# Kernel optimization log

Measured on AMD Instinct MI355X. Metric: run time of the kernel, lower is better.

The kernel has to match this reference:

```python
import jax, jax.numpy as jnp
import numpy as np

D = 192  # volume side; H has shape [D, D, D, 3, 3]


def setup_inputs() -> dict:
    key = jax.random.key(0)
    A = jax.random.normal(key, (D, D, D, 3, 3), dtype=jnp.float32)
    # Hessians are symmetric; the analytic eigen formula assumes symmetry.
    H = 0.5 * (A + jnp.swapaxes(A, -1, -2))
    return {"H": H}


def reference(H):
    # q = trace(H)/3
    q = jnp.trace(H, axis1=-2, axis2=-1) / 3.0
    I = jnp.eye(3, dtype=H.dtype)
    C = H - q[..., None, None] * I  # deviatoric part
    # p = sqrt(||C||_F^2 / 6)
    p = jnp.sqrt(jnp.sum(C * C, axis=(-2, -1)) / 6.0)
    B = C / (p[..., None, None] + 1e-10)
    detB = jnp.linalg.det(B)
    theta = jnp.arccos(jnp.clip(detB / 2.0, -1.0, 1.0)) / 3.0
    two_pi_3 = 2.0 * np.pi / 3.0
    eig = jnp.stack(
        [2.0 * jnp.cos(theta + two_pi_3 * k) * p + q for k in range(3)], axis=-1
    )  # [..., 3]
    return jnp.sort(eig, axis=-1)
```

## Files before the change

kernel.cpp:

```cpp
#include <hip/hip_runtime.h>
#include <math.h>

#define NMAT (192*192*192)

__global__ __launch_bounds__(256) void eig3_kernel(const float* __restrict__ H,
                                                   float* __restrict__ out) {
    __shared__ float lds[256 * 9];
    const int t = threadIdx.x;
    const long long tile = blockIdx.x;
    const long long base = tile * (256LL * 9);

#pragma unroll
    for (int k = 0; k < 9; ++k)
        lds[t + 256 * k] = H[base + t + 256 * k];
    __syncthreads();

    float h[9];
#pragma unroll
    for (int j = 0; j < 9; ++j)
        h[j] = lds[t * 9 + j];
    __syncthreads();

    const float q = (h[0] + h[4] + h[8]) * (1.0f / 3.0f);
    const float c00 = h[0] - q, c01 = h[1],     c02 = h[2];
    const float c10 = h[3],     c11 = h[4] - q, c12 = h[5];
    const float c20 = h[6],     c21 = h[7],     c22 = h[8] - q;
    const float ss = c00*c00 + c01*c01 + c02*c02
                   + c10*c10 + c11*c11 + c12*c12
                   + c20*c20 + c21*c21 + c22*c22;
    const float p = sqrtf(ss * (1.0f / 6.0f));
    const float inv = 1.0f / (p + 1e-10f);
    const float b00 = c00*inv, b01 = c01*inv, b02 = c02*inv;
    const float b10 = c10*inv, b11 = c11*inv, b12 = c12*inv;
    const float b20 = c20*inv, b21 = c21*inv, b22 = c22*inv;
    const float detB = b00*(b11*b22 - b12*b21)
                     - b01*(b10*b22 - b12*b20)
                     + b02*(b10*b21 - b11*b20);
    const float x = fminf(fmaxf(detB * 0.5f, -1.0f), 1.0f);
    const float theta = acosf(x) * (1.0f / 3.0f);
    const float two_pi_3 = 2.09439510239319549f;
    const float e0 = 2.0f * cosf(theta) * p + q;
    const float e1 = 2.0f * cosf(theta + two_pi_3) * p + q;
    const float e2 = 2.0f * cosf(theta + 2.0f * two_pi_3) * p + q;

    const float a  = fminf(e0, e1), b = fmaxf(e0, e1);
    const float hi = fmaxf(b, e2),  c = fminf(b, e2);
    const float lo = fminf(a, c),   mid = fmaxf(a, c);

    lds[t * 3 + 0] = lo;
    lds[t * 3 + 1] = mid;
    lds[t * 3 + 2] = hi;
    __syncthreads();

    const long long obase = tile * (256LL * 3);
#pragma unroll
    for (int k = 0; k < 3; ++k)
        out[obase + t + 256 * k] = lds[t + 256 * k];
}

extern "C" void kernel_launch(void* const* d_in, const int* in_sizes, int n_in,
                              void* d_out, int out_size, void* d_ws, size_t ws_size,
                              hipStream_t stream) {
    const float* H = (const float*)d_in[0];
    float* out = (float*)d_out;
    const int nblocks = NMAT / 256;
    eig3_kernel<<<nblocks, 256, 0, stream>>>(H, out);
}
```

Before: 63.17 us.

## Process four matrices per thread with float4 loads and sincos eigen formula

Each block now handles 1024 matrices, staging input and output through LDS with 128-bit float4 global accesses instead of scalar loads. The three cosines are replaced by one fast __sincosf plus the angle-addition identity, cutting transcendental work. The larger LDS footprint (36KB) and more registers per thread may reduce occupancy, and __sincosf is less accurate than cosf.

```diff
diff --git a/kernel.cpp b/kernel.cpp
--- a/kernel.cpp
+++ b/kernel.cpp
@@ -2,67 +2,82 @@
 #include <math.h>
 
 #define NMAT (192*192*192)
+#define MPB  1024
 
-__global__ __launch_bounds__(256) void eig3_kernel(const float* __restrict__ H,
-                                                   float* __restrict__ out) {
-    __shared__ float lds[256 * 9];
+__global__ __launch_bounds__(256, 4) void eig3_kernel(const float4* __restrict__ H4,
+                                                      float4* __restrict__ out4) {
+    __shared__ float lds[MPB * 9];
+    float4* lds4 = (float4*)lds;
     const int t = threadIdx.x;
-    const long long tile = blockIdx.x;
-    const long long base = tile * (256LL * 9);
+    const long long blk = blockIdx.x;
+
+    const long long ibase = blk * 2304LL;
+#pragma unroll
+    for (int k = 0; k < 9; ++k)
+        lds4[t + 256 * k] = H4[ibase + t + 256 * k];
+    __syncthreads();
+
+    float res[4][3];
+#pragma unroll
+    for (int s = 0; s < 4; ++s) {
+        const int m = t + 256 * s;
+        float h[9];
+#pragma unroll
+        for (int j = 0; j < 9; ++j)
+            h[j] = lds[m * 9 + j];
+
+        const float q = (h[0] + h[4] + h[8]) * (1.0f / 3.0f);
+        const float c00 = h[0] - q, c01 = h[1],     c02 = h[2];
+        const float c10 = h[3],     c11 = h[4] - q, c12 = h[5];
+        const float c20 = h[6],     c21 = h[7],     c22 = h[8] - q;
+        const float ss = c00*c00 + c01*c01 + c02*c02
+                       + c10*c10 + c11*c11 + c12*c12
+                       + c20*c20 + c21*c21 + c22*c22;
+        const float p = sqrtf(ss * (1.0f / 6.0f));
+        const float inv = 1.0f / (p + 1e-10f);
+        const float b00 = c00*inv, b01 = c01*inv, b02 = c02*inv;
+        const float b10 = c10*inv, b11 = c11*inv, b12 = c12*inv;
+        const float b20 = c20*inv, b21 = c21*inv, b22 = c22*inv;
+        const float detB = b00*(b11*b22 - b12*b21)
+                         - b01*(b10*b22 - b12*b20)
+                         + b02*(b10*b21 - b11*b20);
+        const float x = fminf(fmaxf(detB * 0.5f, -1.0f), 1.0f);
+        const float theta = acosf(x) * (1.0f / 3.0f);
+
+        float st, ct;
+        __sincosf(theta, &st, &ct);
+        const float r3 = 1.73205080756887729f;
+        const float e0 = 2.0f * p * ct + q;
+        const float e1 = p * (-ct - r3 * st) + q;
+        const float e2 = p * (-ct + r3 * st) + q;
+
+        const float a  = fminf(e0, e1), b = fmaxf(e0, e1);
+        const float hi = fmaxf(b, e2),  c = fminf(b, e2);
+        const float lo = fminf(a, c),   mid = fmaxf(a, c);
+        res[s][0] = lo; res[s][1] = mid; res[s][2] = hi;
+    }
+    __syncthreads();
 
 #pragma unroll
-    for (int k = 0; k < 9; ++k)
-        lds[t + 256 * k] = H[base + t + 256 * k];
+    for (int s = 0; s < 4; ++s) {
+        const int m = t + 256 * s;
+        lds[m * 3 + 0] = res[s][0];
+        lds[m * 3 + 1] = res[s][1];
+        lds[m * 3 + 2] = res[s][2];
+    }
     __syncthreads();
 
-    float h[9];
-#pragma unroll
-    for (int j = 0; j < 9; ++j)
-        h[j] = lds[t * 9 + j];
-    __syncthreads();
-
-    const float q = (h[0] + h[4] + h[8]) * (1.0f / 3.0f);
-    const float c00 = h[0] - q, c01 = h[1],     c02 = h[2];
-    const float c10 = h[3],     c11 = h[4] - q, c12 = h[5];
-    const float c20 = h[6],     c21 = h[7],     c22 = h[8] - q;
-    const float ss = c00*c00 + c01*c01 + c02*c02
-                   + c10*c10 + c11*c11 + c12*c12
-                   + c20*c20 + c21*c21 + c22*c22;
-    const float p = sqrtf(ss * (1.0f / 6.0f));
-    const float inv = 1.0f / (p + 1e-10f);
-    const float b00 = c00*inv, b01 = c01*inv, b02 = c02*inv;
-    const float b10 = c10*inv, b11 = c11*inv, b12 = c12*inv;
-    const float b20 = c20*inv, b21 = c21*inv, b22 = c22*inv;
-    const float detB = b00*(b11*b22 - b12*b21)
-                     - b01*(b10*b22 - b12*b20)
-                     + b02*(b10*b21 - b11*b20);
-    const float x = fminf(fmaxf(detB * 0.5f, -1.0f), 1.0f);
-    const float theta = acosf(x) * (1.0f / 3.0f);
-    const float two_pi_3 = 2.09439510239319549f;
-    const float e0 = 2.0f * cosf(theta) * p + q;
-    const float e1 = 2.0f * cosf(theta + two_pi_3) * p + q;
-    const float e2 = 2.0f * cosf(theta + 2.0f * two_pi_3) * p + q;
-
-    const float a  = fminf(e0, e1), b = fmaxf(e0, e1);
-    const float hi = fmaxf(b, e2),  c = fminf(b, e2);
-    const float lo = fminf(a, c),   mid = fmaxf(a, c);
-
-    lds[t * 3 + 0] = lo;
-    lds[t * 3 + 1] = mid;
-    lds[t * 3 + 2] = hi;
-    __syncthreads();
-
-    const long long obase = tile * (256LL * 3);
+    const long long obase = blk * 768LL;
 #pragma unroll
     for (int k = 0; k < 3; ++k)
-        out[obase + t + 256 * k] = lds[t + 256 * k];
+        out4[obase + t + 256 * k] = lds4[t + 256 * k];
 }
 
 extern "C" void kernel_launch(void* const* d_in, const int* in_sizes, int n_in,
                               void* d_out, int out_size, void* d_ws, size_t ws_size,
                               hipStream_t stream) {
-    const float* H = (const float*)d_in[0];
-    float* out = (float*)d_out;
-    const int nblocks = NMAT / 256;
-    eig3_kernel<<<nblocks, 256, 0, stream>>>(H, out);
+    const float4* H4 = (const float4*)d_in[0];
+    float4* out4 = (float4*)d_out;
+    const int nblocks = NMAT / MPB;
+    eig3_kernel<<<nblocks, 256, 0, stream>>>(H4, out4);
 }
```

After: 64.68 us. 2.4% more time.
